# Performance work log

Hardware: AMD Instinct MI355X
Metric: run time of the kernel (lower is better)

Reference implementation:

```python
import jax, jax.numpy as jnp
import numpy as np

B, T, E, H = 4, 2048, 1024, 16
HD = E // H  # head_dim = 64


def setup_inputs() -> dict:
    key = jax.random.key(0)
    ks = jax.random.split(key, 6)
    s_in = 1.0 / np.sqrt(HD)
    s_e = 1.0 / np.sqrt(E)
    return {
        "x": jax.random.normal(ks[0], (B, T, E), dtype=jnp.float32),
        # per-head qkv linear: weight [H, HD, 3*HD], bias [H, 3*HD]
        "W_qkv": jax.random.uniform(ks[1], (H, HD, 3 * HD), dtype=jnp.float32, minval=-s_in, maxval=s_in),
        "b_qkv": jax.random.uniform(ks[2], (H, 3 * HD), dtype=jnp.float32, minval=-s_in, maxval=s_in),
        # output projection [E, E]
        "W_proj": jax.random.uniform(ks[3], (E, E), dtype=jnp.float32, minval=-s_e, maxval=s_e),
        "b_proj": jax.random.uniform(ks[4], (E,), dtype=jnp.float32, minval=-s_e, maxval=s_e),
    }


def reference(x, W_qkv, b_qkv, W_proj, b_proj):
    b, t, e = x.shape
    h, hd = W_qkv.shape[0], W_qkv.shape[1]
    # Each head consumes its own contiguous slice of the channel dim.
    xh = x.reshape(b, t, h, hd)  # [B,T,H,HD]
    qkv = jnp.einsum("bthd,hde->bthe", xh, W_qkv) + b_qkv  # [B,T,H,3*HD]
    q, k, v = jnp.split(qkv, 3, axis=-1)  # each [B,T,H,HD]
    scale = 1.0 / (hd ** 0.5 + 1e-05)  # matches (embed_dim ** 0.5 + 1e-05) with embed_dim=head_dim
    attn = jnp.einsum("bthd,bshd->bhts", q, k) * scale  # [B,H,T,T]
    causal = jnp.tril(jnp.ones((t, t), dtype=bool))
    attn = jnp.where(causal, attn, -jnp.inf)
    attn = jax.nn.softmax(attn, axis=-1)
    out = jnp.einsum("bhts,bshd->bthd", attn, v).reshape(b, t, e)  # concat heads
    # dropout is identity in eval mode
    return out @ W_proj.T + b_proj
```

## Files before the change

### kernel.cpp

```cpp
#include <hip/hip_runtime.h>
#include <hip/hip_bf16.h>

#define B_ 4
#define T_ 2048
#define E_ 1024
#define H_ 16
#define HD_ 64

typedef __attribute__((ext_vector_type(8))) short bf16x8;
typedef __attribute__((ext_vector_type(4))) float f32x4;
typedef __attribute__((ext_vector_type(16))) float f32x16;

__device__ inline ushort f2b(float f) {
  union { __hip_bfloat16 h; ushort u; } c;
  c.h = __float2bfloat16(f);
  return c.u;
}
__device__ inline short f2bs(float f) {
  union { __hip_bfloat16 h; short s; } c;
  c.h = __float2bfloat16(f);
  return c.s;
}
__device__ inline int cvtpk(float lo, float hi) {
  int r;
  asm("v_cvt_pk_bf16_f32 %0, %1, %2" : "=v"(r) : "v"(lo), "v"(hi));
  return r;
}
__device__ inline f32x16 zero16() {
  f32x16 z;
#pragma unroll
  for (int i = 0; i < 16; ++i) z[i] = 0.0f;
  return z;
}

__device__ inline void gload16(const ushort* gsrc, ushort* lds_uniform_base) {
  __builtin_amdgcn_global_load_lds(
      (const __attribute__((address_space(1))) void*)gsrc,
      (__attribute__((address_space(3))) void*)lds_uniform_base, 16, 0, 0);
}

__global__ __launch_bounds__(256) void cvt_w_kernel(const float* __restrict__ Wq,
                                                    ushort* __restrict__ Wt) {
  int gtid = blockIdx.x * 256 + threadIdx.x;
  int h = gtid / (HD_ * 192);
  int rem = gtid % (HD_ * 192);
  int d = rem / 192;
  int e = rem % 192;
  Wt[h * (192 * HD_) + e * HD_ + d] = f2b(Wq[gtid]);
}

__global__ __launch_bounds__(256) void cvt_wproj_kernel(const float* __restrict__ Wp,
                                                        ushort* __restrict__ Wb) {
  int i = (blockIdx.x * 256 + threadIdx.x) * 4;
  float4 f = *reinterpret_cast<const float4*>(Wp + i);
  ushort4 u;
  u.x = f2b(f.x); u.y = f2b(f.y); u.z = f2b(f.z); u.w = f2b(f.w);
  *reinterpret_cast<ushort4*>(Wb + i) = u;
}

__global__ __launch_bounds__(256) void qkv_kernel(const float* __restrict__ x,
                                                  const ushort* __restrict__ Wt,
                                                  const float* __restrict__ bq,
                                                  ushort* __restrict__ Q,
                                                  ushort* __restrict__ K,
                                                  ushort* __restrict__ Vt) {
  const float SCALE = (1.0f / (8.0f + 1e-5f)) * 1.4426950408889634f;
  int wave = threadIdx.x >> 6, lane = threadIdx.x & 63;
  int lo = lane & 15, hi = lane >> 4;
  int bh = blockIdx.y, b = bh >> 4, h = bh & 15;
  int t0 = blockIdx.x * 64 + wave * 16;

  const float* xr = x + (size_t)(b * T_ + t0 + lo) * E_ + h * HD_;
  bf16x8 af[2];
#pragma unroll
  for (int c = 0; c < 2; ++c) {
    float4 f0 = *reinterpret_cast<const float4*>(xr + c * 32 + hi * 8);
    float4 f1 = *reinterpret_cast<const float4*>(xr + c * 32 + hi * 8 + 4);
    bf16x8 v;
    v[0] = f2bs(f0.x); v[1] = f2bs(f0.y); v[2] = f2bs(f0.z); v[3] = f2bs(f0.w);
    v[4] = f2bs(f1.x); v[5] = f2bs(f1.y); v[6] = f2bs(f1.z); v[7] = f2bs(f1.w);
    af[c] = v;
  }

  const ushort* Wh = Wt + h * (192 * HD_);
#pragma unroll
  for (int nt = 0; nt < 12; ++nt) {
    int n0 = nt * 16;
    bf16x8 bf0 = *reinterpret_cast<const bf16x8*>(Wh + (size_t)(n0 + lo) * HD_ + hi * 8);
    bf16x8 bf1 = *reinterpret_cast<const bf16x8*>(Wh + (size_t)(n0 + lo) * HD_ + 32 + hi * 8);
    f32x4 acc = {0.0f, 0.0f, 0.0f, 0.0f};
    acc = __builtin_amdgcn_mfma_f32_16x16x32_bf16(af[0], bf0, acc, 0, 0, 0);
    acc = __builtin_amdgcn_mfma_f32_16x16x32_bf16(af[1], bf1, acc, 0, 0, 0);

    int which = nt >> 2;
    int hd = (nt & 3) * 16 + lo;
    float bias = bq[h * 192 + n0 + lo];
    if (which < 2) {
      ushort* dst = which == 0 ? Q : K;
      float sc = which == 0 ? SCALE : 1.0f;
#pragma unroll
      for (int r = 0; r < 4; ++r) {
        int t = t0 + hi * 4 + r;
        dst[((size_t)bh * T_ + t) * HD_ + hd] = f2b((acc[r] + bias) * sc);
      }
    } else {
      ushort4 u;
      u.x = f2b(acc[0] + bias);
      u.y = f2b(acc[1] + bias);
      u.z = f2b(acc[2] + bias);
      u.w = f2b(acc[3] + bias);
      int col = t0 + hi * 4 + hd * 8;
      col &= (T_ - 1);
      *reinterpret_cast<ushort4*>(Vt + ((size_t)bh * HD_ + hd) * T_ + col) = u;
    }
  }
}

__global__ __launch_bounds__(512) void attn_kernel(const ushort* __restrict__ Q,
                                                   const ushort* __restrict__ K,
                                                   const ushort* __restrict__ Vt,
                                                   ushort* __restrict__ AO) {
  __shared__ ushort Ks[3][64 * 64];
  __shared__ ushort Vs[3][64 * 64];

  int wave = threadIdx.x >> 6, lane = threadIdx.x & 63;
  int q5 = lane & 31, hi5 = lane >> 5;
  int bh = blockIdx.x, b = bh >> 4, h = bh & 15;
  int y = blockIdx.y;
  int qt = (y < 4) ? (7 - y) : (y - 4);
  int qw = qt * 256 + wave * 32;

  const ushort* Kbh = K + (size_t)bh * T_ * HD_;
  const ushort* Vbh = Vt + (size_t)bh * HD_ * T_;

  bf16x8 qf[4];
#pragma unroll
  for (int ks = 0; ks < 4; ++ks)
    qf[ks] = *reinterpret_cast<const bf16x8*>(
        Q + ((size_t)bh * T_ + qw + q5) * HD_ + ks * 16 + hi5 * 8);

  f32x16 ot[2];
  ot[0] = zero16(); ot[1] = zero16();
  float mreg = -1e30f, lreg = 0.0f;

  int srow = lane >> 3;
  int sch = lane & 7;

  int ntiles = qt * 4 + 4;

#define STAGE(BUF, TILE)                                                        \
  {                                                                             \
    int kt_ = (TILE) << 6;                                                      \
    int row = wave * 8 + srow;                                                  \
    const ushort* gk = Kbh + (size_t)(kt_ + row) * HD_ + ((sch ^ (row & 7)) * 8); \
    gload16(gk, &Ks[BUF][(wave * 8) * 64]);                                     \
    int col = (kt_ + ((sch ^ (row & 7)) + row) * 8) & (T_ - 1);                 \
    const ushort* gv = Vbh + (size_t)row * T_ + col;                            \
    gload16(gv, &Vs[BUF][(wave * 8) * 64]);                                     \
  }

  STAGE(0, 0);
  STAGE(1, 1);

  int cur = 0;
  for (int tile = 0; tile < ntiles; ++tile) {
    int kt = tile << 6;
    asm volatile("s_waitcnt vmcnt(2)" ::: "memory");
    __builtin_amdgcn_s_barrier();
    {
      int pre = (tile + 2 < ntiles) ? tile + 2 : 0;
      int pb = cur + 2; if (pb >= 3) pb -= 3;
      STAGE(pb, pre);
    }

    if (kt <= qw + 31) {
      f32x16 s[2];
#pragma unroll
      for (int g = 0; g < 2; ++g) {
        int krow = g * 32 + q5;
        bf16x8 kf[4];
#pragma unroll
        for (int ks = 0; ks < 4; ++ks)
          kf[ks] = *reinterpret_cast<const bf16x8*>(
              &Ks[cur][krow * 64 + (((2 * ks + hi5) ^ (krow & 7)) * 8)]);
        f32x16 acc = zero16();
        __builtin_amdgcn_s_setprio(1);
#pragma unroll
        for (int ks = 0; ks < 4; ++ks)
          acc = __builtin_amdgcn_mfma_f32_32x32x16_bf16(kf[ks], qf[ks], acc, 0, 0, 0);
        __builtin_amdgcn_s_setprio(0);
        s[g] = acc;
      }
      if (kt + 63 > qw) {
        int q = qw + q5;
#pragma unroll
        for (int g = 0; g < 2; ++g)
#pragma unroll
          for (int r = 0; r < 16; ++r) {
            int key = kt + g * 32 + (r & 3) + 8 * (r >> 2) + 4 * hi5;
            if (key > q) s[g][r] = -1e30f;
          }
      }
      float t8[8];
#pragma unroll
      for (int i = 0; i < 8; ++i)
        t8[i] = fmaxf(fmaxf(s[0][i], s[0][i + 8]), fmaxf(s[1][i], s[1][i + 8]));
      float mx = fmaxf(fmaxf(fmaxf(t8[0], t8[1]), fmaxf(t8[2], t8[3])),
                       fmaxf(fmaxf(t8[4], t8[5]), fmaxf(t8[6], t8[7])));
      mx = fmaxf(mx, __shfl_xor(mx, 32));
      float nm = fmaxf(mreg, mx);
      float alpha = exp2f(mreg - nm);
      mreg = nm;
#pragma unroll
      for (int g = 0; g < 2; ++g)
#pragma unroll
        for (int r = 0; r < 16; ++r)
          s[g][r] = exp2f(s[g][r] - nm);
      float u8[8];
#pragma unroll
      for (int i = 0; i < 8; ++i)
        u8[i] = (s[0][i] + s[0][i + 8]) + (s[1][i] + s[1][i + 8]);
      float rs = ((u8[0] + u8[1]) + (u8[2] + u8[3])) + ((u8[4] + u8[5]) + (u8[6] + u8[7]));
      rs += __shfl_xor(rs, 32);
      lreg = lreg * alpha + rs;
#pragma unroll
      for (int nh = 0; nh < 2; ++nh)
#pragma unroll
        for (int r = 0; r < 16; ++r) ot[nh][r] *= alpha;

      bf16x8 pb4[4];
#pragma unroll
      for (int ks = 0; ks < 4; ++ks) {
        int g = ks >> 1;
        int R0 = 2 * (ks & 1), R1 = R0 + 1;
        int a0w0 = cvtpk(s[g][4 * R0 + 0], s[g][4 * R0 + 1]);
        int a0w1 = cvtpk(s[g][4 * R0 + 2], s[g][4 * R0 + 3]);
        int a1w0 = cvtpk(s[g][4 * R1 + 0], s[g][4 * R1 + 1]);
        int a1w1 = cvtpk(s[g][4 * R1 + 2], s[g][4 * R1 + 3]);
        int pA0w0 = __shfl_xor(a0w0, 32);
        int pA0w1 = __shfl_xor(a0w1, 32);
        int pA1w0 = __shfl_xor(a1w0, 32);
        int pA1w1 = __shfl_xor(a1w1, 32);
        int4 w;
        w.x = hi5 ? pA1w0 : a0w0;
        w.y = hi5 ? pA1w1 : a0w1;
        w.z = hi5 ? a1w0 : pA0w0;
        w.w = hi5 ? a1w1 : pA0w1;
        pb4[ks] = *reinterpret_cast<bf16x8*>(&w);
      }
#pragma unroll
      for (int nh = 0; nh < 2; ++nh) {
        int vrow = nh * 32 + q5;
        bf16x8 vf[4];
#pragma unroll
        for (int ks = 0; ks < 4; ++ks)
          vf[ks] = *reinterpret_cast<const bf16x8*>(
              &Vs[cur][vrow * 64 + (((2 * ks + hi5) ^ (vrow & 7)) * 8)]);
        __builtin_amdgcn_s_setprio(1);
#pragma unroll
        for (int ks = 0; ks < 4; ++ks)
          ot[nh] = __builtin_amdgcn_mfma_f32_32x32x16_bf16(vf[ks], pb4[ks], ot[nh], 0, 0, 0);
        __builtin_amdgcn_s_setprio(0);
      }
    }
    cur = (cur == 2) ? 0 : cur + 1;
  }
#undef STAGE

  float inv = 1.0f / lreg;
  int t = qw + q5;
  ushort* aop = AO + ((size_t)(b * T_ + t) * H_ + h) * HD_;
#pragma unroll
  for (int nh = 0; nh < 2; ++nh)
#pragma unroll
    for (int R = 0; R < 4; ++R) {
      ushort4 u;
      u.x = f2b(ot[nh][4 * R + 0] * inv);
      u.y = f2b(ot[nh][4 * R + 1] * inv);
      u.z = f2b(ot[nh][4 * R + 2] * inv);
      u.w = f2b(ot[nh][4 * R + 3] * inv);
      *reinterpret_cast<ushort4*>(aop + nh * 32 + 8 * R + 4 * hi5) = u;
    }
}

__global__ __launch_bounds__(256) void proj_kernel(const ushort* __restrict__ A,
                                                   const ushort* __restrict__ Wb,
                                                   const float* __restrict__ bias,
                                                   float* __restrict__ out) {
  __shared__ ushort As[2][128 * 32];
  __shared__ ushort Bs[2][128 * 32];
  int tid = threadIdx.x;
  int wave = tid >> 6, lane = tid & 63;
  int lo = lane & 15, hi = lane >> 4;
  int wr = wave >> 1, wc = wave & 1;
  int m0 = blockIdx.y * 128, n0 = blockIdx.x * 128;

  int srow4 = lane >> 2;
  int sch4 = lane & 3;
  int swz = sch4 ^ ((srow4 >> 1) & 3);

#define PSTAGE(BUF, K0)                                                          \
  {                                                                              \
    _Pragma("unroll")                                                            \
    for (int rep = 0; rep < 2; ++rep) {                                          \
      int row = wave * 32 + rep * 16 + srow4;                                    \
      gload16(A + (size_t)(m0 + row) * E_ + (K0) + swz * 8,                      \
              &As[BUF][(wave * 32 + rep * 16) * 32]);                            \
      gload16(Wb + (size_t)(n0 + row) * E_ + (K0) + swz * 8,                     \
              &Bs[BUF][(wave * 32 + rep * 16) * 32]);                            \
    }                                                                            \
  }

  f32x4 acc[4][4] = {};
  PSTAGE(0, 0);
  asm volatile("s_waitcnt vmcnt(0)" ::: "memory");
  __syncthreads();

  int cur = 0;
  for (int k0 = 0; k0 < E_; k0 += 32) {
    int kpre = (k0 + 32) & (E_ - 1);
    PSTAGE(cur ^ 1, kpre);
    bf16x8 af[4], bfr[4];
#pragma unroll
    for (int i = 0; i < 4; ++i) {
      int row = wr * 64 + i * 16 + lo;
      af[i] = *reinterpret_cast<const bf16x8*>(
          &As[cur][row * 32 + ((hi ^ ((row >> 1) & 3)) * 8)]);
    }
#pragma unroll
    for (int j = 0; j < 4; ++j) {
      int row = wc * 64 + j * 16 + lo;
      bfr[j] = *reinterpret_cast<const bf16x8*>(
          &Bs[cur][row * 32 + ((hi ^ ((row >> 1) & 3)) * 8)]);
    }
    __builtin_amdgcn_s_setprio(1);
#pragma unroll
    for (int i = 0; i < 4; ++i)
#pragma unroll
      for (int j = 0; j < 4; ++j)
        acc[i][j] = __builtin_amdgcn_mfma_f32_16x16x32_bf16(af[i], bfr[j], acc[i][j], 0, 0, 0);
    __builtin_amdgcn_s_setprio(0);
    asm volatile("s_waitcnt vmcnt(0)" ::: "memory");
    __syncthreads();
    cur ^= 1;
  }
#undef PSTAGE

#pragma unroll
  for (int i = 0; i < 4; ++i)
#pragma unroll
    for (int r = 0; r < 4; ++r) {
      int mm = m0 + wr * 64 + i * 16 + hi * 4 + r;
      float* orow = out + (size_t)mm * E_ + n0 + wc * 64;
#pragma unroll
      for (int j = 0; j < 4; ++j)
        orow[j * 16 + lo] = acc[i][j][r] + bias[n0 + wc * 64 + j * 16 + lo];
    }
}

extern "C" void kernel_launch(void* const* d_in, const int* in_sizes, int n_in,
                              void* d_out, int out_size, void* d_ws, size_t ws_size,
                              hipStream_t stream) {
  (void)in_sizes; (void)n_in; (void)out_size; (void)ws_size;
  const float* x  = (const float*)d_in[0];
  const float* Wq = (const float*)d_in[1];
  const float* bq = (const float*)d_in[2];
  const float* Wp = (const float*)d_in[3];
  const float* bp = (const float*)d_in[4];
  float* out = (float*)d_out;

  const size_t NQ = (size_t)B_ * H_ * T_ * HD_;
  ushort* ws = (ushort*)d_ws;
  ushort* Q  = ws;
  ushort* K  = ws + NQ;
  ushort* Vt = ws + 2 * NQ;
  ushort* AO = ws + 3 * NQ;
  ushort* Wb = ws + 4 * NQ;
  ushort* Wt = ws + 4 * NQ + (size_t)E_ * E_;

  cvt_w_kernel<<<dim3(768), dim3(256), 0, stream>>>(Wq, Wt);
  cvt_wproj_kernel<<<dim3(1024), dim3(256), 0, stream>>>(Wp, Wb);
  qkv_kernel<<<dim3(T_ / 64, B_ * H_), dim3(256), 0, stream>>>(x, Wt, bq, Q, K, Vt);
  attn_kernel<<<dim3(B_ * H_, 8), dim3(512), 0, stream>>>(Q, K, Vt, AO);
  proj_kernel<<<dim3(E_ / 128, (B_ * T_) / 128), dim3(256), 0, stream>>>(AO, Wb, bp, out);
}
```

Measured before the change: 151.7 us.

## Pair-process attention tiles with 4-buffer ring and triple-buffer projection GEMM

The attention loop now handles two K/V tiles per iteration. It uses a 4-slot LDS ring, issuing prefetches for the next pair and paying one barrier per two tiles instead of one per tile. The projection GEMM moves from double buffering, with a full vmcnt(0) wait and syncthreads every K step, to a 3-stage ring with a partial vmcnt wait and a single barrier per step. Both changes aim to cut synchronization stalls and overlap global loads with MFMA work. The cost is more LDS per block: 64KB for attention and 48KB for projection. That may reduce blocks per CU, and the attention kernel now waits for all outstanding loads at each pair boundary.

```diff
diff --git a/kernel.cpp b/kernel.cpp
--- a/kernel.cpp
+++ b/kernel.cpp
@@ -120,8 +120,8 @@
                                                    const ushort* __restrict__ K,
                                                    const ushort* __restrict__ Vt,
                                                    ushort* __restrict__ AO) {
-  __shared__ ushort Ks[3][64 * 64];
-  __shared__ ushort Vs[3][64 * 64];
+  __shared__ ushort Ks[4][64 * 64];
+  __shared__ ushort Vs[4][64 * 64];
 
   int wave = threadIdx.x >> 6, lane = threadIdx.x & 63;
   int q5 = lane & 31, hi5 = lane >> 5;
@@ -159,111 +159,116 @@
     gload16(gv, &Vs[BUF][(wave * 8) * 64]);                                     \
   }
 
+  auto compute_tile = [&](int tile, int buf) {
+    int kt = tile << 6;
+    if (kt > qw + 31) return;
+    f32x16 s[2];
+#pragma unroll
+    for (int g = 0; g < 2; ++g) {
+      int krow = g * 32 + q5;
+      bf16x8 kf[4];
+#pragma unroll
+      for (int ks = 0; ks < 4; ++ks)
+        kf[ks] = *reinterpret_cast<const bf16x8*>(
+            &Ks[buf][krow * 64 + (((2 * ks + hi5) ^ (krow & 7)) * 8)]);
+      f32x16 acc = zero16();
+      __builtin_amdgcn_s_setprio(1);
+#pragma unroll
+      for (int ks = 0; ks < 4; ++ks)
+        acc = __builtin_amdgcn_mfma_f32_32x32x16_bf16(kf[ks], qf[ks], acc, 0, 0, 0);
+      __builtin_amdgcn_s_setprio(0);
+      s[g] = acc;
+    }
+    if (kt + 63 > qw) {
+      int q = qw + q5;
+#pragma unroll
+      for (int g = 0; g < 2; ++g)
+#pragma unroll
+        for (int r = 0; r < 16; ++r) {
+          int key = kt + g * 32 + (r & 3) + 8 * (r >> 2) + 4 * hi5;
+          if (key > q) s[g][r] = -1e30f;
+        }
+    }
+    float t8[8];
+#pragma unroll
+    for (int i = 0; i < 8; ++i)
+      t8[i] = fmaxf(fmaxf(s[0][i], s[0][i + 8]), fmaxf(s[1][i], s[1][i + 8]));
+    float mx = fmaxf(fmaxf(fmaxf(t8[0], t8[1]), fmaxf(t8[2], t8[3])),
+                     fmaxf(fmaxf(t8[4], t8[5]), fmaxf(t8[6], t8[7])));
+    mx = fmaxf(mx, __shfl_xor(mx, 32));
+    float nm = fmaxf(mreg, mx);
+    float alpha = exp2f(mreg - nm);
+    mreg = nm;
+#pragma unroll
+    for (int g = 0; g < 2; ++g)
+#pragma unroll
+      for (int r = 0; r < 16; ++r)
+        s[g][r] = exp2f(s[g][r] - nm);
+    float u8[8];
+#pragma unroll
+    for (int i = 0; i < 8; ++i)
+      u8[i] = (s[0][i] + s[0][i + 8]) + (s[1][i] + s[1][i + 8]);
+    float rs = ((u8[0] + u8[1]) + (u8[2] + u8[3])) + ((u8[4] + u8[5]) + (u8[6] + u8[7]));
+    rs += __shfl_xor(rs, 32);
+    lreg = lreg * alpha + rs;
+#pragma unroll
+    for (int nh = 0; nh < 2; ++nh)
+#pragma unroll
+      for (int r = 0; r < 16; ++r) ot[nh][r] *= alpha;
+
+    bf16x8 pb4[4];
+#pragma unroll
+    for (int ks = 0; ks < 4; ++ks) {
+      int g = ks >> 1;
+      int R0 = 2 * (ks & 1), R1 = R0 + 1;
+      int a0w0 = cvtpk(s[g][4 * R0 + 0], s[g][4 * R0 + 1]);
+      int a0w1 = cvtpk(s[g][4 * R0 + 2], s[g][4 * R0 + 3]);
+      int a1w0 = cvtpk(s[g][4 * R1 + 0], s[g][4 * R1 + 1]);
+      int a1w1 = cvtpk(s[g][4 * R1 + 2], s[g][4 * R1 + 3]);
+      int pA0w0 = __shfl_xor(a0w0, 32);
+      int pA0w1 = __shfl_xor(a0w1, 32);
+      int pA1w0 = __shfl_xor(a1w0, 32);
+      int pA1w1 = __shfl_xor(a1w1, 32);
+      int4 w;
+      w.x = hi5 ? pA1w0 : a0w0;
+      w.y = hi5 ? pA1w1 : a0w1;
+      w.z = hi5 ? a1w0 : pA0w0;
+      w.w = hi5 ? a1w1 : pA0w1;
+      pb4[ks] = *reinterpret_cast<bf16x8*>(&w);
+    }
+#pragma unroll
+    for (int nh = 0; nh < 2; ++nh) {
+      int vrow = nh * 32 + q5;
+      bf16x8 vf[4];
+#pragma unroll
+      for (int ks = 0; ks < 4; ++ks)
+        vf[ks] = *reinterpret_cast<const bf16x8*>(
+            &Vs[buf][vrow * 64 + (((2 * ks + hi5) ^ (vrow & 7)) * 8)]);
+      __builtin_amdgcn_s_setprio(1);
+#pragma unroll
+      for (int ks = 0; ks < 4; ++ks)
+        ot[nh] = __builtin_amdgcn_mfma_f32_32x32x16_bf16(vf[ks], pb4[ks], ot[nh], 0, 0, 0);
+      __builtin_amdgcn_s_setprio(0);
+    }
+  };
+
   STAGE(0, 0);
   STAGE(1, 1);
 
-  int cur = 0;
-  for (int tile = 0; tile < ntiles; ++tile) {
-    int kt = tile << 6;
-    asm volatile("s_waitcnt vmcnt(2)" ::: "memory");
+  int npairs = ntiles >> 1;
+  for (int p = 0; p < npairs; ++p) {
+    int t0 = 2 * p, t1 = 2 * p + 1;
+    asm volatile("s_waitcnt vmcnt(0)" ::: "memory");
     __builtin_amdgcn_s_barrier();
     {
-      int pre = (tile + 2 < ntiles) ? tile + 2 : 0;
-      int pb = cur + 2; if (pb >= 3) pb -= 3;
-      STAGE(pb, pre);
-    }
-
-    if (kt <= qw + 31) {
-      f32x16 s[2];
-#pragma unroll
-      for (int g = 0; g < 2; ++g) {
-        int krow = g * 32 + q5;
-        bf16x8 kf[4];
-#pragma unroll
-        for (int ks = 0; ks < 4; ++ks)
-          kf[ks] = *reinterpret_cast<const bf16x8*>(
-              &Ks[cur][krow * 64 + (((2 * ks + hi5) ^ (krow & 7)) * 8)]);
-        f32x16 acc = zero16();
-        __builtin_amdgcn_s_setprio(1);
-#pragma unroll
-        for (int ks = 0; ks < 4; ++ks)
-          acc = __builtin_amdgcn_mfma_f32_32x32x16_bf16(kf[ks], qf[ks], acc, 0, 0, 0);
-        __builtin_amdgcn_s_setprio(0);
-        s[g] = acc;
-      }
-      if (kt + 63 > qw) {
-        int q = qw + q5;
-#pragma unroll
-        for (int g = 0; g < 2; ++g)
-#pragma unroll
-          for (int r = 0; r < 16; ++r) {
-            int key = kt + g * 32 + (r & 3) + 8 * (r >> 2) + 4 * hi5;
-            if (key > q) s[g][r] = -1e30f;
-          }
-      }
-      float t8[8];
-#pragma unroll
-      for (int i = 0; i < 8; ++i)
-        t8[i] = fmaxf(fmaxf(s[0][i], s[0][i + 8]), fmaxf(s[1][i], s[1][i + 8]));
-      float mx = fmaxf(fmaxf(fmaxf(t8[0], t8[1]), fmaxf(t8[2], t8[3])),
-                       fmaxf(fmaxf(t8[4], t8[5]), fmaxf(t8[6], t8[7])));
-      mx = fmaxf(mx, __shfl_xor(mx, 32));
-      float nm = fmaxf(mreg, mx);
-      float alpha = exp2f(mreg - nm);
-      mreg = nm;
-#pragma unroll
-      for (int g = 0; g < 2; ++g)
-#pragma unroll
-        for (int r = 0; r < 16; ++r)
-          s[g][r] = exp2f(s[g][r] - nm);
-      float u8[8];
-#pragma unroll
-      for (int i = 0; i < 8; ++i)
-        u8[i] = (s[0][i] + s[0][i + 8]) + (s[1][i] + s[1][i + 8]);
-      float rs = ((u8[0] + u8[1]) + (u8[2] + u8[3])) + ((u8[4] + u8[5]) + (u8[6] + u8[7]));
-      rs += __shfl_xor(rs, 32);
-      lreg = lreg * alpha + rs;
-#pragma unroll
-      for (int nh = 0; nh < 2; ++nh)
-#pragma unroll
-        for (int r = 0; r < 16; ++r) ot[nh][r] *= alpha;
-
-      bf16x8 pb4[4];
-#pragma unroll
-      for (int ks = 0; ks < 4; ++ks) {
-        int g = ks >> 1;
-        int R0 = 2 * (ks & 1), R1 = R0 + 1;
-        int a0w0 = cvtpk(s[g][4 * R0 + 0], s[g][4 * R0 + 1]);
-        int a0w1 = cvtpk(s[g][4 * R0 + 2], s[g][4 * R0 + 3]);
-        int a1w0 = cvtpk(s[g][4 * R1 + 0], s[g][4 * R1 + 1]);
-        int a1w1 = cvtpk(s[g][4 * R1 + 2], s[g][4 * R1 + 3]);
-        int pA0w0 = __shfl_xor(a0w0, 32);
-        int pA0w1 = __shfl_xor(a0w1, 32);
-        int pA1w0 = __shfl_xor(a1w0, 32);
-        int pA1w1 = __shfl_xor(a1w1, 32);
-        int4 w;
-        w.x = hi5 ? pA1w0 : a0w0;
-        w.y = hi5 ? pA1w1 : a0w1;
-        w.z = hi5 ? a1w0 : pA0w0;
-        w.w = hi5 ? a1w1 : pA0w1;
-        pb4[ks] = *reinterpret_cast<bf16x8*>(&w);
-      }
-#pragma unroll
-      for (int nh = 0; nh < 2; ++nh) {
-        int vrow = nh * 32 + q5;
-        bf16x8 vf[4];
-#pragma unroll
-        for (int ks = 0; ks < 4; ++ks)
-          vf[ks] = *reinterpret_cast<const bf16x8*>(
-              &Vs[cur][vrow * 64 + (((2 * ks + hi5) ^ (vrow & 7)) * 8)]);
-        __builtin_amdgcn_s_setprio(1);
-#pragma unroll
-        for (int ks = 0; ks < 4; ++ks)
-          ot[nh] = __builtin_amdgcn_mfma_f32_32x32x16_bf16(vf[ks], pb4[ks], ot[nh], 0, 0, 0);
-        __builtin_amdgcn_s_setprio(0);
-      }
-    }
-    cur = (cur == 2) ? 0 : cur + 1;
+      int pr0 = t0 + 2, pr1 = t0 + 3;
+      int s0 = (pr0 < ntiles) ? pr0 : 0;
+      int s1 = (pr1 < ntiles) ? pr1 : 0;
+      STAGE(pr0 & 3, s0);
+      STAGE(pr1 & 3, s1);
+    }
+    compute_tile(t0, t0 & 3);
+    compute_tile(t1, t1 & 3);
   }
 #undef STAGE
 
@@ -287,8 +292,8 @@
                                                    const ushort* __restrict__ Wb,
                                                    const float* __restrict__ bias,
                                                    float* __restrict__ out) {
-  __shared__ ushort As[2][128 * 32];
-  __shared__ ushort Bs[2][128 * 32];
+  __shared__ ushort As[3][128 * 32];
+  __shared__ ushort Bs[3][128 * 32];
   int tid = threadIdx.x;
   int wave = tid >> 6, lane = tid & 63;
   int lo = lane & 15, hi = lane >> 4;
@@ -313,13 +318,16 @@
 
   f32x4 acc[4][4] = {};
   PSTAGE(0, 0);
-  asm volatile("s_waitcnt vmcnt(0)" ::: "memory");
-  __syncthreads();
-
-  int cur = 0;
-  for (int k0 = 0; k0 < E_; k0 += 32) {
-    int kpre = (k0 + 32) & (E_ - 1);
-    PSTAGE(cur ^ 1, kpre);
+  PSTAGE(1, 32);
+
+  for (int kk = 0; kk < 32; ++kk) {
+    asm volatile("s_waitcnt vmcnt(4)" ::: "memory");
+    __builtin_amdgcn_s_barrier();
+    {
+      int kpre = ((kk + 2) << 5) & (E_ - 1);
+      PSTAGE((kk + 2) % 3, kpre);
+    }
+    int cur = kk % 3;
     bf16x8 af[4], bfr[4];
 #pragma unroll
     for (int i = 0; i < 4; ++i) {
@@ -340,9 +348,6 @@
       for (int j = 0; j < 4; ++j)
         acc[i][j] = __builtin_amdgcn_mfma_f32_16x16x32_bf16(af[i], bfr[j], acc[i][j], 0, 0, 0);
     __builtin_amdgcn_s_setprio(0);
-    asm volatile("s_waitcnt vmcnt(0)" ::: "memory");
-    __syncthreads();
-    cur ^= 1;
   }
 #undef PSTAGE
 
```

After: 152.9 us. About the same (+0.8%).
